# Performance work log

Hardware: AMD Instinct MI355X
Metric: run time of the kernel (lower is better)

## Reference

```python
import math
import jax, jax.numpy as jnp
import numpy as np

COULOMB = 14.399645478425668  # eV*Angstrom / e^2


def setup_inputs() -> dict:
    key = jax.random.key(0)
    k0, k1, k2, k3, k4 = jax.random.split(key, 5)
    B, n, F, S = 128, 512, 64, 4  # molecules, atoms/molecule, feat dim, n species
    N = B * n
    node_features = jax.random.normal(k0, (N, F), dtype=jnp.float32)
    pos = jax.random.normal(k1, (N, 3), dtype=jnp.float32) * 5.0  # spread atoms out
    atom_type = jax.random.randint(k2, (N,), 0, S)
    total_charge = jnp.zeros((B, 1), dtype=jnp.float32)
    chi_weight = jax.random.normal(k3, (F, 1), dtype=jnp.float32) / np.float32(np.sqrt(F))
    hardness_param = jnp.ones((S,), dtype=jnp.float32)
    sigma = 0.3 + 0.5 * jax.random.uniform(k4, (S,), dtype=jnp.float32)  # covalent radii
    return dict(node_features=node_features, pos=pos, atom_type=atom_type,
                total_charge=total_charge, chi_weight=chi_weight,
                hardness_param=hardness_param, sigma=sigma, n_per_mol=n)


def reference(node_features, pos, atom_type, total_charge, chi_weight,
              hardness_param, sigma, n_per_mol):
    n = n_per_mol
    N, F = node_features.shape
    B = N // n

    feats = node_features.reshape(B, n, F)
    pos_b = pos.reshape(B, n, 3)
    sp = atom_type.reshape(B, n)

    chi = (feats @ chi_weight)[..., 0]                      # [B, n] electronegativity
    hard = jnp.square(hardness_param)[sp]                   # [B, n]
    sig = sigma[sp]                                         # [B, n]

    # pairwise distances within each molecule (diag masked for safe divide)
    diff = pos_b[:, :, None, :] - pos_b[:, None, :, :]      # [B, n, n, 3]
    d2 = jnp.sum(diff * diff, axis=-1)
    eye = jnp.eye(n, dtype=pos.dtype)
    d = jnp.sqrt(jnp.where(eye, 1.0, d2))                   # [B, n, n]

    gamma = jnp.sqrt(sig[:, :, None] ** 2 + sig[:, None, :] ** 2)
    off = COULOMB * jax.lax.erf(d / (math.sqrt(2.0) * gamma)) / d
    diag = hard + COULOMB / (math.sqrt(math.pi) * sig)      # [B, n]
    coeffs = off * (1.0 - eye) + eye * diag[:, :, None]     # [B, n, n]

    # augmented Qeq system with charge-conservation Lagrange multiplier
    A = jnp.ones((B, n + 1, n + 1), dtype=coeffs.dtype)
    A = A.at[:, :n, :n].set(coeffs)
    A = A.at[:, n, n].set(0.0)
    rhs = jnp.concatenate([-chi, total_charge], axis=1)     # [B, n+1]
    sol = jnp.linalg.solve(A, rhs[..., None])[..., 0]
    q = sol[:, :n]                                          # [B, n] charges

    # E = sum_{i<j} C_ij q_i q_j + sum_i (chi_i q_i + 0.5 diag_i q_i^2)
    #   = 0.5 q^T C q + chi . q   (C includes diagonal)
    e_qeq = 0.5 * jnp.einsum('bi,bij,bj->b', q, coeffs, q) + jnp.sum(chi * q, axis=1)
    return e_qeq[:, None], q.reshape(N, 1)
```

## Files before the change

### kernel.cpp

```cpp
#include <hip/hip_runtime.h>
#include <math.h>

#define NA 512
#define NN (NA*NA)
#define COULOMB 14.399645478425668f
#define SQRT_PI 1.7724538509055160273f

#define TB 320
#define TS 192
#define TSTR 193

typedef float v2f __attribute__((ext_vector_type(2)));

__device__ __forceinline__ float rl(float x, int lane) {
    return __int_as_float(__builtin_amdgcn_readlane(__float_as_int(x), lane));
}

__device__ __forceinline__ float pair_val(float dx, float dy, float dz,
                                          float s2i, float s2k) {
    float d2 = dx*dx + dy*dy + dz*dz;
    float rinv = rsqrtf(d2);
    return COULOMB * erff(d2 * rinv * rsqrtf(2.f * (s2i + s2k))) * rinv;
}

__global__ void k_pre(const float* __restrict__ feats, const float* __restrict__ w,
                      const int* __restrict__ type, const float* __restrict__ hard,
                      const float* __restrict__ sigma,
                      float* __restrict__ chi, float* __restrict__ diag,
                      float* __restrict__ sigA,
                      float* __restrict__ r1, float* __restrict__ r2, int N) {
    __shared__ float wl[64];
    int tid = threadIdx.x;
    if (tid < 64) wl[tid] = w[tid];
    __syncthreads();
    int i = blockIdx.x * 256 + tid;
    if (i >= N) return;
    const float4* fp = (const float4*)(feats + (size_t)i * 64);
    float acc = 0.f;
#pragma unroll
    for (int q = 0; q < 16; q++) {
        float4 v = fp[q];
        acc += v.x * wl[4*q] + v.y * wl[4*q+1] + v.z * wl[4*q+2] + v.w * wl[4*q+3];
    }
    chi[i] = acc;
    r1[i] = acc;
    r2[i] = 1.0f;
    int t = type[i];
    float s = sigma[t];
    float h = hard[t];
    sigA[i] = s;
    diag[i] = h * h + COULOMB / (SQRT_PI * s);
}

__global__ void __launch_bounds__(256, 1) k_panel(const float* __restrict__ pos,
                                                  const float* __restrict__ sigA,
                                                  const float* __restrict__ diagA,
                                                  float* __restrict__ C,
                                                  float* __restrict__ r1,
                                                  float* __restrict__ r2, const int j) {
    const int q = blockIdx.x;
    const int b = blockIdx.y;
    float* __restrict__ Cb = C + (size_t)b * NN;
    const int jb = j * 64;
    const int m = NA - jb - 64;
    const int tid = threadIdx.x;
    __shared__ float D[64 * 65];
    __shared__ float DT[64 * 64];
    __shared__ float invd[64];
    __shared__ float y1s[64], y2s[64];
    __shared__ float px[NA], py[NA], pz[NA], s2s[NA];

    if (j == 0) {
#pragma unroll
        for (int e = 0; e < 2; e++) {
            int i = e * 256 + tid;
            px[i] = pos[((size_t)b * NA + i) * 3 + 0];
            py[i] = pos[((size_t)b * NA + i) * 3 + 1];
            pz[i] = pos[((size_t)b * NA + i) * 3 + 2];
            float s = sigA[b * NA + i];
            s2s[i] = s * s;
        }
        __syncthreads();
    }

#pragma unroll
    for (int e = 0; e < 16; e++) {
        int f = e * 256 + tid;
        int rr = f >> 6, cc = f & 63;
        float v;
        if (j == 0) {
            if (rr == cc) v = diagA[b * NA + rr];
            else v = pair_val(px[rr]-px[cc], py[rr]-py[cc], pz[rr]-pz[cc], s2s[rr], s2s[cc]);
        } else {
            v = Cb[(size_t)(jb + rr) * NA + jb + cc];
        }
        D[rr * 65 + cc] = v;
    }

    const int h = m >> 1;
    const int r0 = q ? h : 0;
    const int nr = q ? (m - h) : h;
    const int r = tid - 32;
    const bool hasrow = (r >= 0 && r < nr);
    const int grow = jb + 64 + r0 + r;
    float rv[64];
    if (hasrow) {
        if (j == 0) {
#pragma unroll
            for (int k = 0; k < 64; k++)
                rv[k] = pair_val(px[grow]-px[k], py[grow]-py[k], pz[grow]-pz[k],
                                 s2s[grow], s2s[k]);
        } else {
            const float4* rp = (const float4*)(Cb + (size_t)grow * NA + jb);
#pragma unroll
            for (int qq = 0; qq < 16; qq++) {
                float4 v = rp[qq];
                rv[4*qq] = v.x; rv[4*qq+1] = v.y; rv[4*qq+2] = v.z; rv[4*qq+3] = v.w;
            }
        }
    }
    __syncthreads();

    if (tid < 64) {
        const int t = tid;
        float cl[64];
#pragma unroll
        for (int i = 0; i < 64; i++) cl[i] = (i >= t) ? D[i * 65 + t] : D[t * 65 + i];
#pragma unroll
        for (int k = 0; k < 64; k++) {
            float pivot = rl(cl[k], k);
            float invp = 1.0f / pivot;
            float factor = (t > k) ? (cl[k] * invp) : 0.0f;
#pragma unroll
            for (int i = k + 1; i < 64; i++) {
                float bc = rl(cl[i], k);
                cl[i] -= bc * factor;
            }
        }
        float rs = 1.0f / sqrtf(cl[t]);
        invd[t] = rs;
#pragma unroll
        for (int i = 0; i < 64; i++)
            if (i >= t) D[i * 65 + t] = cl[i] * rs;

        float v1 = r1[(size_t)b * NA + jb + t];
        float v2 = r2[(size_t)b * NA + jb + t];
#pragma unroll
        for (int k = 0; k < 64; k++) {
            float rsk = rl(rs, k);
            float y1k = rl(v1, k) * rsk;
            float y2k = rl(v2, k) * rsk;
            if (t == k) {
                y1s[t] = y1k; y2s[t] = y2k;
                if (q == 0) {
                    r1[(size_t)b * NA + jb + t] = y1k;
                    r2[(size_t)b * NA + jb + t] = y2k;
                }
            }
            float lv = (t > k) ? D[t * 65 + k] : 0.f;
            v1 -= lv * y1k;
            v2 -= lv * y2k;
        }
    }
    __syncthreads();

#pragma unroll
    for (int e = 0; e < 16; e++) {
        int f = e * 256 + tid;
        int row = f >> 6, cc = f & 63;
        float v = D[row * 65 + cc];
        DT[row * 64 + cc] = (cc < row) ? v : 0.f;
        if (q == 0 && cc <= row) Cb[(size_t)(jb + row) * NA + jb + cc] = v;
    }
    __syncthreads();

    if (hasrow) {
#pragma unroll
        for (int k = 0; k < 64; k++) {
            float acc = rv[k];
            const float4* Lr = (const float4*)(DT + k * 64);
            const int k4 = k >> 2;
#pragma unroll
            for (int t4 = 0; t4 < k4; t4++) {
                float4 Lv = Lr[t4];
                acc -= Lv.x * rv[4*t4] + Lv.y * rv[4*t4+1] + Lv.z * rv[4*t4+2] + Lv.w * rv[4*t4+3];
            }
#pragma unroll
            for (int tt = k4 * 4; tt < k; tt++) acc -= DT[k * 64 + tt] * rv[tt];
            rv[k] = acc * invd[k];
        }
        float4* rp = (float4*)(Cb + (size_t)grow * NA + jb);
#pragma unroll
        for (int qq = 0; qq < 16; qq++)
            rp[qq] = make_float4(rv[4*qq], rv[4*qq+1], rv[4*qq+2], rv[4*qq+3]);

        float a1 = 0.f, a2 = 0.f;
#pragma unroll
        for (int k = 0; k < 64; k++) {
            a1 = fmaf(rv[k], y1s[k], a1);
            a2 = fmaf(rv[k], y2s[k], a2);
        }
        r1[(size_t)b * NA + grow] -= a1;
        r2[(size_t)b * NA + grow] -= a2;
    }
}

template<bool GEN>
__global__ void __launch_bounds__(256, 2) k_trail(float* __restrict__ C,
                                                  const float* __restrict__ pos,
                                                  const float* __restrict__ sigA,
                                                  const float* __restrict__ diagA,
                                                  const int j) {
    const int b = blockIdx.y;
    float* __restrict__ Cb = C + (size_t)b * NN;
    const int jb = j * 64;
    const int m = NA - jb - 64;
    int t = blockIdx.x;
    int RI = 0;
    while (t >= RI + 1) { t -= RI + 1; RI++; }
    const int RJ = t;
    const int RB = RI * 128, CB = RJ * 128;
    const int vr = min(128, m - RB);
    const int vc = min(128, m - CB);
    const int tid = threadIdx.x;
    const int rg = tid >> 4, cg = tid & 15;

    __shared__ float As[128 * 66];
    __shared__ float Bs[128 * 66];

    v2f ac2[8][8];

    if (GEN) {
        __shared__ float pAx[128], pAy[128], pAz[128], sA[128], dA[128];
        __shared__ float pBx[128], pBy[128], pBz[128], sB[128];
        if (tid < 128) {
            if (RB + tid < m) {
                int ga = b * NA + jb + 64 + RB + tid;
                pAx[tid] = pos[(size_t)ga * 3 + 0];
                pAy[tid] = pos[(size_t)ga * 3 + 1];
                pAz[tid] = pos[(size_t)ga * 3 + 2];
                float s = sigA[ga]; sA[tid] = s * s;
                dA[tid] = diagA[ga];
            }
        } else {
            int u = tid - 128;
            if (CB + u < m) {
                int gb = b * NA + jb + 64 + CB + u;
                pBx[u] = pos[(size_t)gb * 3 + 0];
                pBy[u] = pos[(size_t)gb * 3 + 1];
                pBz[u] = pos[(size_t)gb * 3 + 2];
                float s = sigA[gb]; sB[u] = s * s;
            }
        }
        __syncthreads();
#pragma unroll
        for (int rr = 0; rr < 8; rr++) {
            int row = rg * 8 + rr;
#pragma unroll
            for (int cc = 0; cc < 8; cc++) {
                int col = cg + 16 * cc;
                float iv;
                if (RB + row == CB + col)
                    iv = dA[row];
                else
                    iv = pair_val(pAx[row]-pBx[col], pAy[row]-pBy[col],
                                  pAz[row]-pBz[col], sA[row], sB[col]);
                ac2[rr][cc].x = iv;
                ac2[rr][cc].y = 0.f;
            }
        }
        __syncthreads();
    } else {
        const int GRB = jb + 64 + RB, GCB = jb + 64 + CB;
#pragma unroll
        for (int rr = 0; rr < 8; rr++) {
            int row = rg * 8 + rr;
#pragma unroll
            for (int cc = 0; cc < 8; cc++) {
                int col = cg + 16 * cc;
                ac2[rr][cc].x = (row < vr && col < vc)
                    ? Cb[(size_t)(GRB + row) * NA + GCB + col] : 0.f;
                ac2[rr][cc].y = 0.f;
            }
        }
    }

    const float* Pan = Cb + (size_t)(jb + 64) * NA + jb;
#pragma unroll
    for (int e = 0; e < 8; e++) {
        int f = e * 256 + tid;
        int row = f >> 4, s = f & 15;
        float4 v = make_float4(0.f, 0.f, 0.f, 0.f);
        if (row < vr) v = *(const float4*)(Pan + (size_t)(RB + row) * NA + s * 4);
        As[row * 66 + s * 4 + 0] = v.x;
        As[row * 66 + s * 4 + 1] = v.y;
        As[row * 66 + s * 4 + 2] = v.z;
        As[row * 66 + s * 4 + 3] = v.w;
        float4 u = make_float4(0.f, 0.f, 0.f, 0.f);
        if (row < vc) u = *(const float4*)(Pan + (size_t)(CB + row) * NA + s * 4);
        Bs[row * 66 + s * 4 + 0] = u.x;
        Bs[row * 66 + s * 4 + 1] = u.y;
        Bs[row * 66 + s * 4 + 2] = u.z;
        Bs[row * 66 + s * 4 + 3] = u.w;
    }
    __syncthreads();

#pragma unroll 2
    for (int k = 0; k < 64; k += 2) {
        v2f ai2[8], bj2[8];
#pragma unroll
        for (int rr = 0; rr < 8; rr++)
            ai2[rr] = *(const v2f*)&As[(rg * 8 + rr) * 66 + k];
#pragma unroll
        for (int cc = 0; cc < 8; cc++)
            bj2[cc] = *(const v2f*)&Bs[(cg + 16 * cc) * 66 + k];
#pragma unroll
        for (int rr = 0; rr < 8; rr++)
#pragma unroll
            for (int cc = 0; cc < 8; cc++) {
                ac2[rr][cc].x = fmaf(-ai2[rr].x, bj2[cc].x, ac2[rr][cc].x);
                ac2[rr][cc].y = fmaf(-ai2[rr].y, bj2[cc].y, ac2[rr][cc].y);
            }
    }

    const int GRB = jb + 64 + RB, GCB = jb + 64 + CB;
#pragma unroll
    for (int rr = 0; rr < 8; rr++) {
        int row = rg * 8 + rr;
        if (row < vr) {
#pragma unroll
            for (int cc = 0; cc < 8; cc++) {
                int col = cg + 16 * cc;
                if (col < vc)
                    Cb[(size_t)(GRB + row) * NA + GCB + col] = ac2[rr][cc].x + ac2[rr][cc].y;
            }
        }
    }
}

__global__ void __launch_bounds__(512, 1) k_tail(float* __restrict__ C,
                                                 float* __restrict__ r1,
                                                 float* __restrict__ r2) {
    const int b = blockIdx.x;
    float* __restrict__ Cb = C + (size_t)b * NN;
    const int tid = threadIdx.x;
    __shared__ float T[TS * TSTR];
    __shared__ float invd[64], y1s[64], y2s[64];

    for (int f = tid; f < TS * TS; f += 512) {
        int row = f / TS, c = f - row * TS;
        T[row * TSTR + c] = Cb[(size_t)(TB + row) * NA + TB + c];
    }
    __syncthreads();

#pragma unroll 1
    for (int p = 0; p < 3; p++) {
        const int pb = p * 64;
        const int msub = TS - pb - 64;

        if (tid < 64) {
            const int t = tid;
            float cl[64];
#pragma unroll
            for (int i = 0; i < 64; i++)
                cl[i] = (i >= t) ? T[(pb + i) * TSTR + pb + t]
                                 : T[(pb + t) * TSTR + pb + i];
#pragma unroll
            for (int k = 0; k < 64; k++) {
                float pivot = rl(cl[k], k);
                float invp = 1.0f / pivot;
                float factor = (t > k) ? (cl[k] * invp) : 0.0f;
#pragma unroll
                for (int i = k + 1; i < 64; i++) {
                    float bc = rl(cl[i], k);
                    cl[i] -= bc * factor;
                }
            }
            float rs = 1.0f / sqrtf(cl[t]);
            invd[t] = rs;
#pragma unroll
            for (int i = 0; i < 64; i++) {
                float lv = cl[i] * rs;
                if (i >= t) T[(pb + i) * TSTR + pb + t] = lv;
                if (i > t)  T[(pb + t) * TSTR + pb + i] = lv;
            }
            float v1 = r1[(size_t)b * NA + TB + pb + t];
            float v2 = r2[(size_t)b * NA + TB + pb + t];
#pragma unroll
            for (int k = 0; k < 64; k++) {
                float rsk = rl(rs, k);
                float y1k = rl(v1, k) * rsk;
                float y2k = rl(v2, k) * rsk;
                if (t == k) {
                    y1s[t] = y1k; y2s[t] = y2k;
                    r1[(size_t)b * NA + TB + pb + t] = y1k;
                    r2[(size_t)b * NA + TB + pb + t] = y2k;
                }
                float lv = (t > k) ? T[(pb + t) * TSTR + pb + k] : 0.f;
                v1 -= lv * y1k;
                v2 -= lv * y2k;
            }
        }
        __syncthreads();

        if (msub > 0) {
            if (tid < msub) {
                const int row_l = pb + 64 + tid;
                float rv[64];
#pragma unroll
                for (int k = 0; k < 64; k++) rv[k] = T[row_l * TSTR + pb + k];
#pragma unroll
                for (int k = 0; k < 64; k++) {
                    float yk = rv[k] * invd[k];
                    rv[k] = yk;
                    const float* LTrow = &T[(pb + k) * TSTR + pb];
#pragma unroll
                    for (int i = k + 1; i < 64; i++)
                        rv[i] -= LTrow[i] * yk;
                }
#pragma unroll
                for (int k = 0; k < 64; k++) T[row_l * TSTR + pb + k] = rv[k];
                float a1 = 0.f, a2 = 0.f;
#pragma unroll
                for (int k = 0; k < 64; k++) {
                    a1 = fmaf(rv[k], y1s[k], a1);
                    a2 = fmaf(rv[k], y2s[k], a2);
                }
                r1[(size_t)b * NA + TB + row_l] -= a1;
                r2[(size_t)b * NA + TB + row_l] -= a2;
            }
            __syncthreads();

            const int rbase = pb + 64;
            if (p == 0) {
                const int rg = tid >> 4, cg = tid & 15;
                float acc[4][8];
#pragma unroll
                for (int rr = 0; rr < 4; rr++)
#pragma unroll
                    for (int cc = 0; cc < 8; cc++)
                        acc[rr][cc] = T[(rbase + rg * 4 + rr) * TSTR + rbase + cg * 8 + cc];
#pragma unroll 4
                for (int k = 0; k < 64; k++) {
                    float ai[4], bj[8];
#pragma unroll
                    for (int rr = 0; rr < 4; rr++)
                        ai[rr] = T[(rbase + rg * 4 + rr) * TSTR + pb + k];
#pragma unroll
                    for (int cc = 0; cc < 8; cc++)
                        bj[cc] = T[(rbase + cg * 8 + cc) * TSTR + pb + k];
#pragma unroll
                    for (int rr = 0; rr < 4; rr++)
#pragma unroll
                        for (int cc = 0; cc < 8; cc++)
                            acc[rr][cc] = fmaf(-ai[rr], bj[cc], acc[rr][cc]);
                }
#pragma unroll
                for (int rr = 0; rr < 4; rr++)
#pragma unroll
                    for (int cc = 0; cc < 8; cc++)
                        T[(rbase + rg * 4 + rr) * TSTR + rbase + cg * 8 + cc] = acc[rr][cc];
            } else {
                const int rg = tid >> 4, cg = tid & 15;
                float acc[2][4];
#pragma unroll
                for (int rr = 0; rr < 2; rr++)
#pragma unroll
                    for (int cc = 0; cc < 4; cc++)
                        acc[rr][cc] = T[(rbase + rg * 2 + rr) * TSTR + rbase + cg * 4 + cc];
#pragma unroll 4
                for (int k = 0; k < 64; k++) {
                    float ai[2], bj[4];
#pragma unroll
                    for (int rr = 0; rr < 2; rr++)
                        ai[rr] = T[(rbase + rg * 2 + rr) * TSTR + pb + k];
#pragma unroll
                    for (int cc = 0; cc < 4; cc++)
                        bj[cc] = T[(rbase + cg * 4 + cc) * TSTR + pb + k];
#pragma unroll
                    for (int rr = 0; rr < 2; rr++)
#pragma unroll
                        for (int cc = 0; cc < 4; cc++)
                            acc[rr][cc] = fmaf(-ai[rr], bj[cc], acc[rr][cc]);
                }
#pragma unroll
                for (int rr = 0; rr < 2; rr++)
#pragma unroll
                    for (int cc = 0; cc < 4; cc++)
                        T[(rbase + rg * 2 + rr) * TSTR + rbase + cg * 4 + cc] = acc[rr][cc];
            }
        }
        __syncthreads();
    }

    for (int f = tid; f < TS * TS; f += 512) {
        int row = f / TS, c = f - row * TS;
        Cb[(size_t)(TB + row) * NA + TB + c] = T[row * TSTR + c];
    }
}

__global__ void __launch_bounds__(512, 1) k_back(const float* __restrict__ C,
                                                 float* __restrict__ r1g,
                                                 float* __restrict__ r2g) {
    const int b = blockIdx.x;
    const int rhs = blockIdx.y;
    const float* Cb = C + (size_t)b * NN;
    const int tid = threadIdx.x;
    __shared__ float D[64 * 65];
    __shared__ float r[NA];
    __shared__ float pb[4][NA];

    float* rg = rhs ? r2g : r1g;
    r[tid] = rg[(size_t)b * NA + tid];

    const int ii = tid & 127;
    const int gg = tid >> 7;
    for (int j = 7; j >= 0; j--) {
        const int jb = j * 64;
        __syncthreads();
#pragma unroll
        for (int e = 0; e < 8; e++) {
            int f = e * 512 + tid;
            int row = f >> 6, cc = f & 63;
            D[row * 65 + cc] = Cb[(size_t)(jb + row) * NA + jb + cc];
        }
        __syncthreads();
        if (tid < 64) {
            float val = r[jb + tid];
            float idg = 1.0f / D[tid * 65 + tid];
#pragma unroll
            for (int k = 63; k >= 0; k--) {
                float xk = rl(val, k) * rl(idg, k);
                if (tid == k) r[jb + k] = xk;
                float lv = (tid < k) ? D[k * 65 + tid] : 0.f;
                val -= lv * xk;
            }
        }
        __syncthreads();
        if (jb > 0) {
            const int nf4 = jb >> 2;
            float4 s1 = make_float4(0.f, 0.f, 0.f, 0.f);
            if (ii < nf4) {
#pragma unroll
                for (int gq = 0; gq < 16; gq++) {
                    int g = jb + gg * 16 + gq;
                    float x1 = r[g];
                    float4 Lv = *(const float4*)(Cb + (size_t)g * NA + ii * 4);
                    s1.x += Lv.x * x1; s1.y += Lv.y * x1; s1.z += Lv.z * x1; s1.w += Lv.w * x1;
                }
            }
            *(float4*)(&pb[gg][ii * 4]) = s1;
            __syncthreads();
            if (tid < jb)
                r[tid] -= pb[0][tid] + pb[1][tid] + pb[2][tid] + pb[3][tid];
        }
    }
    __syncthreads();

    rg[(size_t)b * NA + tid] = r[tid];
}

__global__ void __launch_bounds__(512, 1) k_final(const float* __restrict__ x1,
                                                  const float* __restrict__ x2,
                                                  const float* __restrict__ chiA,
                                                  const float* __restrict__ Qtot,
                                                  float* __restrict__ out, int B) {
    const int b = blockIdx.x;
    const int tid = threadIdx.x;
    __shared__ float red[16];
    __shared__ float muS;

    float v1 = x1[(size_t)b * NA + tid];
    float v2 = x2[(size_t)b * NA + tid];

    float s1p = v1, s2p = v2;
#pragma unroll
    for (int off = 1; off < 64; off <<= 1) {
        s1p += __shfl_xor(s1p, off);
        s2p += __shfl_xor(s2p, off);
    }
    if ((tid & 63) == 0) { red[tid >> 6] = s1p; red[8 + (tid >> 6)] = s2p; }
    __syncthreads();
    if (tid == 0) {
        float s1 = 0.f, s2 = 0.f;
#pragma unroll
        for (int wv = 0; wv < 8; wv++) { s1 += red[wv]; s2 += red[8 + wv]; }
        muS = -(Qtot[b] + s1) / s2;
    }
    __syncthreads();
    float mu = muS;
    float qv = -v1 - mu * v2;
    out[B + (size_t)b * NA + tid] = qv;

    float eacc = chiA[b * NA + tid] * qv;
#pragma unroll
    for (int off = 1; off < 64; off <<= 1) eacc += __shfl_xor(eacc, off);
    __syncthreads();
    if ((tid & 63) == 0) red[tid >> 6] = eacc;
    __syncthreads();
    if (tid == 0) {
        float e = 0.f;
#pragma unroll
        for (int wv = 0; wv < 8; wv++) e += red[wv];
        out[b] = 0.5f * e - 0.5f * mu * Qtot[b];
    }
}

extern "C" void kernel_launch(void* const* d_in, const int* in_sizes, int n_in,
                              void* d_out, int out_size, void* d_ws, size_t ws_size,
                              hipStream_t stream) {
    const int B = in_sizes[3];
    const int N = in_sizes[2];
    const float* feats = (const float*)d_in[0];
    const float* pos   = (const float*)d_in[1];
    const int*   type  = (const int*)d_in[2];
    const float* Qt    = (const float*)d_in[3];
    const float* w     = (const float*)d_in[4];
    const float* hard  = (const float*)d_in[5];
    const float* sig   = (const float*)d_in[6];
    float* out = (float*)d_out;
    float* ws  = (float*)d_ws;

    float* C    = ws;
    float* chi  = ws + (size_t)B * NN;
    float* diag = chi + N;
    float* sigA = diag + N;
    float* r1   = sigA + N;
    float* r2   = r1 + N;

    k_pre<<<(N + 255) / 256, 256, 0, stream>>>(feats, w, type, hard, sig,
                                               chi, diag, sigA, r1, r2, N);

    static const int tilesJ[5] = {10, 6, 6, 3, 3};
    for (int j = 0; j < 5; j++) {
        k_panel<<<dim3(2, B), 256, 0, stream>>>(pos, sigA, diag, C, r1, r2, j);
        if (j == 0)
            k_trail<true><<<dim3(tilesJ[j], B), 256, 0, stream>>>(C, pos, sigA, diag, j);
        else
            k_trail<false><<<dim3(tilesJ[j], B), 256, 0, stream>>>(C, pos, sigA, diag, j);
    }
    k_tail<<<B, 512, 0, stream>>>(C, r1, r2);
    k_back<<<dim3(B, 2), 512, 0, stream>>>(C, r1, r2);
    k_final<<<B, 512, 0, stream>>>(r1, r2, chi, Qt, out, B);
}
```

Measured before the change: 719.4 us.

## Use split-fp16 MFMA for trailing Cholesky/LU updates after first panel

Replaces the FP32 scalar trailing-matrix update for panels 1-4 with a new kernel that splits each panel value into high and low fp16 halves and accumulates three 32x32x16 MFMA products into fp32. The first panel's generate-and-update kernel keeps the scalar path. The goal is to move the rank-64 update GEMM onto matrix cores and cut ALU time. In exchange, the three-term fp16 split loses some precision versus fp32, and fp16 range limits could hurt accuracy for large coefficient values.

```diff
diff --git a/kernel.cpp b/kernel.cpp
--- a/kernel.cpp
+++ b/kernel.cpp
@@ -10,7 +10,11 @@
 #define TS 192
 #define TSTR 193
 
+#define FST 72
+
 typedef float v2f __attribute__((ext_vector_type(2)));
+typedef _Float16 half8 __attribute__((ext_vector_type(8)));
+typedef float floatx16 __attribute__((ext_vector_type(16)));
 
 __device__ __forceinline__ float rl(float x, int lane) {
     return __int_as_float(__builtin_amdgcn_readlane(__float_as_int(x), lane));
@@ -205,16 +209,14 @@
     }
 }
 
-template<bool GEN>
-__global__ void __launch_bounds__(256, 2) k_trail(float* __restrict__ C,
-                                                  const float* __restrict__ pos,
-                                                  const float* __restrict__ sigA,
-                                                  const float* __restrict__ diagA,
-                                                  const int j) {
+__global__ void __launch_bounds__(256, 2) k_trail0(float* __restrict__ C,
+                                                   const float* __restrict__ pos,
+                                                   const float* __restrict__ sigA,
+                                                   const float* __restrict__ diagA) {
     const int b = blockIdx.y;
     float* __restrict__ Cb = C + (size_t)b * NN;
-    const int jb = j * 64;
-    const int m = NA - jb - 64;
+    const int jb = 0;
+    const int m = NA - 64;
     int t = blockIdx.x;
     int RI = 0;
     while (t >= RI + 1) { t -= RI + 1; RI++; }
@@ -230,7 +232,7 @@
 
     v2f ac2[8][8];
 
-    if (GEN) {
+    {
         __shared__ float pAx[128], pAy[128], pAz[128], sA[128], dA[128];
         __shared__ float pBx[128], pBy[128], pBz[128], sB[128];
         if (tid < 128) {
@@ -270,19 +272,6 @@
             }
         }
         __syncthreads();
-    } else {
-        const int GRB = jb + 64 + RB, GCB = jb + 64 + CB;
-#pragma unroll
-        for (int rr = 0; rr < 8; rr++) {
-            int row = rg * 8 + rr;
-#pragma unroll
-            for (int cc = 0; cc < 8; cc++) {
-                int col = cg + 16 * cc;
-                ac2[rr][cc].x = (row < vr && col < vc)
-                    ? Cb[(size_t)(GRB + row) * NA + GCB + col] : 0.f;
-                ac2[rr][cc].y = 0.f;
-            }
-        }
     }
 
     const float* Pan = Cb + (size_t)(jb + 64) * NA + jb;
@@ -338,6 +327,115 @@
     }
 }
 
+__global__ void __launch_bounds__(256, 2) k_trailm(float* __restrict__ C, const int j) {
+    const int b = blockIdx.y;
+    float* __restrict__ Cb = C + (size_t)b * NN;
+    const int jb = j * 64;
+    const int m = NA - jb - 64;
+    int t = blockIdx.x;
+    int RI = 0;
+    while (t >= RI + 1) { t -= RI + 1; RI++; }
+    const int RJ = t;
+    const int RB = RI * 128, CB = RJ * 128;
+    const int vr = min(128, m - RB);
+    const int vc = min(128, m - CB);
+    const int tid = threadIdx.x;
+    const int lane = tid & 63;
+    const int wv = tid >> 6;
+    const int tr0 = (wv >> 1) * 2;
+    const int tc0 = (wv & 1) * 2;
+    const int lcol = lane & 31;
+    const int lrhi = (lane >> 5) * 4;
+    const int kfo = (lane >> 5) * 8;
+
+    __shared__ __attribute__((aligned(16))) _Float16 Ash[128 * FST];
+    __shared__ __attribute__((aligned(16))) _Float16 Asl[128 * FST];
+    __shared__ __attribute__((aligned(16))) _Float16 Bsh[128 * FST];
+    __shared__ __attribute__((aligned(16))) _Float16 Bsl[128 * FST];
+
+    floatx16 acc[2][2];
+
+    const int GRB = jb + 64 + RB, GCB = jb + 64 + CB;
+#pragma unroll
+    for (int a = 0; a < 2; a++)
+#pragma unroll
+        for (int bb = 0; bb < 2; bb++)
+#pragma unroll
+            for (int r = 0; r < 16; r++) {
+                int row = (tr0 + a) * 32 + (r & 3) + 8 * (r >> 2) + lrhi;
+                int col = (tc0 + bb) * 32 + lcol;
+                acc[a][bb][r] = (row < vr && col < vc)
+                    ? Cb[(size_t)(GRB + row) * NA + GCB + col] : 0.f;
+            }
+
+    const float* Pan = Cb + (size_t)(jb + 64) * NA + jb;
+#pragma unroll
+    for (int e = 0; e < 8; e++) {
+        int f = e * 256 + tid;
+        int row = f >> 4, s = f & 15;
+        float4 v = make_float4(0.f, 0.f, 0.f, 0.f);
+        if (row < vr) v = *(const float4*)(Pan + (size_t)(RB + row) * NA + s * 4);
+        float av[4] = {v.x, v.y, v.z, v.w};
+#pragma unroll
+        for (int c = 0; c < 4; c++) {
+            float nx = -av[c];
+            _Float16 hh = (_Float16)nx;
+            _Float16 ll = (_Float16)(nx - (float)hh);
+            Ash[row * FST + s * 4 + c] = hh;
+            Asl[row * FST + s * 4 + c] = ll;
+        }
+        float4 u = make_float4(0.f, 0.f, 0.f, 0.f);
+        if (row < vc) u = *(const float4*)(Pan + (size_t)(CB + row) * NA + s * 4);
+        float bv[4] = {u.x, u.y, u.z, u.w};
+#pragma unroll
+        for (int c = 0; c < 4; c++) {
+            float x = bv[c];
+            _Float16 hh = (_Float16)x;
+            _Float16 ll = (_Float16)(x - (float)hh);
+            Bsh[row * FST + s * 4 + c] = hh;
+            Bsl[row * FST + s * 4 + c] = ll;
+        }
+    }
+    __syncthreads();
+
+#pragma unroll
+    for (int ks = 0; ks < 4; ks++) {
+        half8 Ah[2], Al[2], Bh[2], Bl[2];
+#pragma unroll
+        for (int a = 0; a < 2; a++) {
+            int off = ((tr0 + a) * 32 + lcol) * FST + ks * 16 + kfo;
+            Ah[a] = *(const half8*)&Ash[off];
+            Al[a] = *(const half8*)&Asl[off];
+        }
+#pragma unroll
+        for (int bb = 0; bb < 2; bb++) {
+            int off = ((tc0 + bb) * 32 + lcol) * FST + ks * 16 + kfo;
+            Bh[bb] = *(const half8*)&Bsh[off];
+            Bl[bb] = *(const half8*)&Bsl[off];
+        }
+#pragma unroll
+        for (int a = 0; a < 2; a++)
+#pragma unroll
+            for (int bb = 0; bb < 2; bb++) {
+                acc[a][bb] = __builtin_amdgcn_mfma_f32_32x32x16_f16(Ah[a], Bh[bb], acc[a][bb], 0, 0, 0);
+                acc[a][bb] = __builtin_amdgcn_mfma_f32_32x32x16_f16(Ah[a], Bl[bb], acc[a][bb], 0, 0, 0);
+                acc[a][bb] = __builtin_amdgcn_mfma_f32_32x32x16_f16(Al[a], Bh[bb], acc[a][bb], 0, 0, 0);
+            }
+    }
+
+#pragma unroll
+    for (int a = 0; a < 2; a++)
+#pragma unroll
+        for (int bb = 0; bb < 2; bb++)
+#pragma unroll
+            for (int r = 0; r < 16; r++) {
+                int row = (tr0 + a) * 32 + (r & 3) + 8 * (r >> 2) + lrhi;
+                int col = (tc0 + bb) * 32 + lcol;
+                if (row < vr && col < vc)
+                    Cb[(size_t)(GRB + row) * NA + GCB + col] = acc[a][bb][r];
+            }
+}
+
 __global__ void __launch_bounds__(512, 1) k_tail(float* __restrict__ C,
                                                  float* __restrict__ r1,
                                                  float* __restrict__ r2) {
@@ -635,9 +733,9 @@
     for (int j = 0; j < 5; j++) {
         k_panel<<<dim3(2, B), 256, 0, stream>>>(pos, sigA, diag, C, r1, r2, j);
         if (j == 0)
-            k_trail<true><<<dim3(tilesJ[j], B), 256, 0, stream>>>(C, pos, sigA, diag, j);
+            k_trail0<<<dim3(tilesJ[j], B), 256, 0, stream>>>(C, pos, sigA, diag);
         else
-            k_trail<false><<<dim3(tilesJ[j], B), 256, 0, stream>>>(C, pos, sigA, diag, j);
+            k_trailm<<<dim3(tilesJ[j], B), 256, 0, stream>>>(C, j);
     }
     k_tail<<<B, 512, 0, stream>>>(C, r1, r2);
     k_back<<<dim3(B, 2), 512, 0, stream>>>(C, r1, r2);
```

New measurement: 1.068 ms (median of 2 runs). +48.4%, slower.
